# Kernel tuning notes

Measured on AMD Instinct MI355X. Metric: run time of the kernel, lower is better.

Reference implementation:

```python
import jax, jax.numpy as jnp
import numpy as np

N = 50000   # nodes per domain graph
E = 800000  # edges per graph (avg degree 16)
IN = 512    # in_feats
H = 256     # n_hidden
C = 10      # n_classes
ALPHA = 1.0


def setup_inputs() -> dict:
    key = jax.random.key(0)
    ks = jax.random.split(key, 16)
    inp = {
        "features_s": jax.random.normal(ks[0], (N, IN), jnp.float32),
        "labels_s": jax.random.randint(ks[1], (N,), 0, C, jnp.int32),
        "features_t": jax.random.normal(ks[2], (N, IN), jnp.float32),
        "src_s": jax.random.randint(ks[3], (E,), 0, N, jnp.int32),
        "dst_s": jax.random.randint(ks[4], (E,), 0, N, jnp.int32),
        "src_t": jax.random.randint(ks[5], (E,), 0, N, jnp.int32),
        "dst_t": jax.random.randint(ks[6], (E,), 0, N, jnp.int32),
        # GraphConv layer 0: in_feats -> n_hidden (glorot-ish init)
        "W0": jax.random.normal(ks[7], (IN, H), jnp.float32) / np.float32(np.sqrt(IN)),
        "b0": jnp.zeros((H,), jnp.float32),
        # GraphConv layer 1: n_hidden -> n_hidden
        "W1": jax.random.normal(ks[8], (H, H), jnp.float32) / np.float32(np.sqrt(H)),
        "b1": jnp.zeros((H,), jnp.float32),
        # fc head: n_hidden -> n_classes
        "Wfc": jax.random.normal(ks[9], (H, C), jnp.float32) / np.float32(np.sqrt(H)),
        "bfc": jnp.zeros((C,), jnp.float32),
        # JS discriminator: (n_hidden*n_layers + n_classes) -> 2
        "Wd": jax.random.normal(ks[10], (H * 2 + C, 2), jnp.float32) / np.float32(np.sqrt(H * 2 + C)),
        "bd": jnp.zeros((2,), jnp.float32),
    }
    return inp


def _gconv(x, src, dst, W, b, n):
    # DGL GraphConv with norm='both': out = D_in^{-1/2} A D_out^{-1/2} x W + b, then relu.
    ones = jnp.ones(src.shape, x.dtype)
    deg_out = jax.ops.segment_sum(ones, src, num_segments=n)
    deg_in = jax.ops.segment_sum(ones, dst, num_segments=n)
    norm_src = jnp.maximum(deg_out, 1.0) ** -0.5   # [n]
    norm_dst = jnp.maximum(deg_in, 1.0) ** -0.5    # [n]
    h = (x * norm_src[:, None]) @ W                # [n, out] (mult-first: row scaling commutes)
    agg = jax.ops.segment_sum(h[src], dst, num_segments=n)  # gather-scatter SpMM
    return jax.nn.relu(agg * norm_dst[:, None] + b)


def reference(features_s, labels_s, features_t, src_s, dst_s, src_t, dst_t,
              W0, b0, W1, b1, Wfc, bfc, Wd, bd):
    # dropout omitted (eval-mode determinism)
    hs, ht = features_s, features_t
    s_list, t_list = [], []
    for (W, b) in ((W0, b0), (W1, b1)):
        hs = _gconv(hs, src_s, dst_s, W, b, N)
        ht = _gconv(ht, src_t, dst_t, W, b, N)
        s_list.append(hs)
        t_list.append(ht)
    logits_s = hs @ Wfc + bfc
    logits_t = ht @ Wfc + bfc
    s_list.append(logits_s)
    t_list.append(logits_t)

    # class loss: nll over log_softmax
    logp = jax.nn.log_softmax(logits_s, axis=-1)
    class_loss = -jnp.mean(jnp.take_along_axis(logp, labels_s[:, None].astype(jnp.int32), axis=1))

    # JS domain loss with gradient-reversal (identity in forward)
    s_f = jnp.concatenate(s_list, axis=1)  # [N, 2H+C]
    t_f = jnp.concatenate(t_list, axis=1)
    both = jnp.concatenate([s_f, t_f], axis=0)  # [2N, 2H+C]
    rev = -ALPHA * both + jax.lax.stop_gradient((1.0 + ALPHA) * both)  # GRL trick
    dlogits = rev @ Wd + bd
    dlogp = jax.nn.log_softmax(dlogits, axis=-1)
    dlabels = jnp.concatenate([jnp.zeros((N,), jnp.int32), jnp.ones((N,), jnp.int32)])
    domain_loss = -jnp.mean(jnp.take_along_axis(dlogp, dlabels[:, None], axis=1))

    return class_loss + 0.01 * domain_loss
```

## Files before the change

### kernel.cpp

```cpp
#include <hip/hip_runtime.h>
#include <cstdint>
#include <cstddef>

#define NN 50000
#define NNP 50016
#define EE 800000
#define INF 512
#define HH  256
#define CC  10
#define NB2 391
#define NTB 782
#define GB64 782
#define SPMM_BLOCKS 1600
#define HBIN 6250
#define HRNG 8
#define HSUB 32
#define SCAP 1536
#define ZROW NN
#define CAST_TOT (INF * HH + HH * HH + 16 * HH + 16 * HH)

using bfrag = __attribute__((ext_vector_type(8))) __bf16;
using f32x4 = __attribute__((ext_vector_type(4))) float;
using f32x2 = __attribute__((ext_vector_type(2))) float;

__device__ inline unsigned short f2bf(float x) {
    unsigned u = __builtin_bit_cast(unsigned, x);
    unsigned r = u + 0x7FFFu + ((u >> 16) & 1u);
    return (unsigned short)(r >> 16);
}
__device__ inline float bf2f(unsigned short h) {
    return __builtin_bit_cast(float, (unsigned)h << 16);
}

__device__ inline void gload_lds16(const void* gsrc, void* ldst) {
    __builtin_amdgcn_global_load_lds(
        (const __attribute__((address_space(1))) void*)gsrc,
        (__attribute__((address_space(3))) void*)ldst, 16, 0, 0);
}

__global__ void k_cast_all(const float* __restrict__ W0, const float* __restrict__ W1,
                           const float* __restrict__ Wfc, const float* __restrict__ Wd,
                           ushort* __restrict__ W0t, ushort* __restrict__ W1t,
                           ushort* __restrict__ Wt1, ushort* __restrict__ Wt2) {
    int idx = blockIdx.x * blockDim.x + threadIdx.x;
    if (idx < INF * HH) {
        int n = idx / INF, k = idx % INF;
        W0t[idx] = f2bf(W0[(size_t)k * HH + n]);
    } else if (idx < INF * HH + HH * HH) {
        int j = idx - INF * HH;
        int n = j / HH, k = j % HH;
        W1t[j] = f2bf(W1[(size_t)k * HH + n]);
    } else if (idx < INF * HH + HH * HH + 16 * HH) {
        int j = idx - INF * HH - HH * HH;
        int n = j >> 8, k = j & 255;
        float v = 0.f;
        if (n < 10)       v = Wfc[(size_t)k * 10 + n];
        else if (n < 12)  v = Wd[(size_t)(HH + k) * 2 + (n - 10)];
        Wt1[j] = f2bf(v);
    } else if (idx < CAST_TOT) {
        int j = idx - INF * HH - HH * HH - 16 * HH;
        int n = j >> 8, k = j & 255;
        float v = (n < 2) ? Wd[(size_t)k * 2 + n] : 0.f;
        Wt2[j] = f2bf(v);
    }
}

__global__ __launch_bounds__(256) void k_deghist(
        const int* __restrict__ src_s, const int* __restrict__ dst_s,
        const int* __restrict__ src_t, const int* __restrict__ dst_t,
        ushort* __restrict__ pcnt) {
    __shared__ int hist[HBIN];
    const int task = blockIdx.x >> 5;
    const int sub  = blockIdx.x & 31;
    const int arr = task >> 3, range = task & 7;
    const int* p = (arr == 0) ? src_s : (arr == 1) ? dst_s : (arr == 2) ? src_t : dst_t;
    const int4* p4 = reinterpret_cast<const int4*>(p);
    const int lo = range * HBIN;
    for (int j = threadIdx.x; j < HBIN; j += 256) hist[j] = 0;
    __syncthreads();
    for (int i = sub * 256 + (int)threadIdx.x; i < EE / 4; i += HSUB * 256) {
        int4 v = p4[i];
        int a0 = v.x - lo, a1 = v.y - lo, a2 = v.z - lo, a3 = v.w - lo;
        if ((unsigned)a0 < (unsigned)HBIN) atomicAdd(&hist[a0], 1);
        if ((unsigned)a1 < (unsigned)HBIN) atomicAdd(&hist[a1], 1);
        if ((unsigned)a2 < (unsigned)HBIN) atomicAdd(&hist[a2], 1);
        if ((unsigned)a3 < (unsigned)HBIN) atomicAdd(&hist[a3], 1);
    }
    __syncthreads();
    ushort* out = pcnt + ((size_t)task * HSUB + sub) * HBIN;
    for (int j = threadIdx.x; j < HBIN; j += 256) out[j] = (ushort)hist[j];
}

__global__ void k_degsum(const ushort* __restrict__ pcnt, int* __restrict__ cnt) {
    int g = blockIdx.x * blockDim.x + threadIdx.x;
    if (g >= 4 * NN) return;
    int arr = g / NN;
    int node = g - arr * NN;
    int range = node / HBIN;
    int j = node - range * HBIN;
    const ushort* p = pcnt + ((size_t)(arr * HRNG + range) * HSUB) * HBIN + j;
    int s = 0;
    #pragma unroll
    for (int k = 0; k < HSUB; ++k) s += p[(size_t)k * HBIN];
    cnt[g] = s;
}

__global__ void k_scan_blk(const int* __restrict__ cnt, int* __restrict__ off,
                           int* __restrict__ btot) {
    __shared__ int wsum[4];
    int tid = threadIdx.x, lane = tid & 63, wid = tid >> 6;
    int i = blockIdx.x * 256 + tid;
    int v = 0;
    if (i < 2 * NN) v = (i < NN) ? cnt[NN + i] : cnt[2 * NN + i];
    int s = v;
    #pragma unroll
    for (int o = 1; o < 64; o <<= 1) {
        int t = __shfl_up(s, o, 64);
        if (lane >= o) s += t;
    }
    if (lane == 63) wsum[wid] = s;
    __syncthreads();
    if (tid == 0) {
        int a = 0;
        #pragma unroll
        for (int w2 = 0; w2 < 4; ++w2) { int t = wsum[w2]; wsum[w2] = a; a += t; }
        btot[blockIdx.x] = a;
    }
    __syncthreads();
    if (i < 2 * NN) off[i] = wsum[wid] + s - v;
}

__global__ void k_scan_tops(const int* __restrict__ btot, int* __restrict__ bbase,
                            int* __restrict__ off) {
    __shared__ int wsum[8];
    int tid = threadIdx.x, lane = tid & 63, wid = tid >> 6;
    int v = (tid < NB2) ? btot[tid] : 0;
    int s = v;
    #pragma unroll
    for (int o = 1; o < 64; o <<= 1) {
        int t = __shfl_up(s, o, 64);
        if (lane >= o) s += t;
    }
    if (lane == 63) wsum[wid] = s;
    __syncthreads();
    if (tid == 0) {
        int a = 0;
        #pragma unroll
        for (int w2 = 0; w2 < 8; ++w2) { int t = wsum[w2]; wsum[w2] = a; a += t; }
        off[2 * NN] = a;
    }
    __syncthreads();
    if (tid < NB2) bbase[tid] = wsum[wid] + s - v;
}

__global__ void k_scan_fin(int* __restrict__ off, const int* __restrict__ bbase,
                           const int* __restrict__ cnt,
                           float* __restrict__ ns, float* __restrict__ nd,
                           ushort* __restrict__ y2,
                           const ushort* __restrict__ pcnt, int* __restrict__ base2) {
    if (blockIdx.x == 0) {
        #pragma unroll
        for (int j = 0; j < 2; ++j) {
            int idx = j * 256 + (int)threadIdx.x;
            int gg = idx >> 8, grp = (idx >> 5) & 7, c = idx & 31;
            y2[(((size_t)gg * 8 + grp) * NNP + ZROW) * 32 + c] = 0;
        }
    }
    int i = blockIdx.x * blockDim.x + threadIdx.x;
    if (i >= 2 * NN) return;
    int o = off[i] + bbase[i >> 8];
    off[i] = o;
    int co = (i < NN) ? cnt[i] : cnt[NN + i];
    int ci = (i < NN) ? cnt[NN + i] : cnt[2 * NN + i];
    ns[i] = 1.0f / sqrtf(fmaxf((float)co, 1.0f));
    nd[i] = 1.0f / sqrtf(fmaxf((float)ci, 1.0f));
    int g = (i < NN) ? 0 : 1;
    int node = i - g * NN;
    int range = node / HBIN;
    int bin = node - range * HBIN;
    int arr = g ? 3 : 1;
    const ushort* p = pcnt + ((size_t)(arr * HRNG + range) * HSUB) * HBIN + bin;
    int* b = base2 + ((size_t)(g * HRNG + range) * HSUB) * HBIN + bin;
    int run = o;
    #pragma unroll
    for (int s = 0; s < HSUB; ++s) {
        b[(size_t)s * HBIN] = run;
        run += p[(size_t)s * HBIN];
    }
}

__global__ __launch_bounds__(256) void k_fill3(
        const int* __restrict__ src_s, const int* __restrict__ dst_s,
        const int* __restrict__ src_t, const int* __restrict__ dst_t,
        const int* __restrict__ base2, int* __restrict__ csr_src) {
    __shared__ int cur[HBIN];
    const int combo = blockIdx.x & 15;
    const int sub = blockIdx.x >> 4;
    const int g = combo >> 3, range = combo & 7;
    const int4* d4 = reinterpret_cast<const int4*>(g ? dst_t : dst_s);
    const int4* s4 = reinterpret_cast<const int4*>(g ? src_t : src_s);
    const int lo = range * HBIN;
    const int* b = base2 + (size_t)combo * HSUB * HBIN + (size_t)sub * HBIN;
    for (int j = threadIdx.x; j < HBIN; j += 256) cur[j] = b[j];
    __syncthreads();
    for (int i = sub * 256 + (int)threadIdx.x; i < EE / 4; i += HSUB * 256) {
        int4 d = d4[i];
        int b0 = d.x - lo, b1 = d.y - lo, b2 = d.z - lo, b3 = d.w - lo;
        bool o0 = (unsigned)b0 < (unsigned)HBIN;
        bool o1 = (unsigned)b1 < (unsigned)HBIN;
        bool o2 = (unsigned)b2 < (unsigned)HBIN;
        bool o3 = (unsigned)b3 < (unsigned)HBIN;
        if (o0 | o1 | o2 | o3) {
            int4 s = s4[i];
            if (o0) csr_src[atomicAdd(&cur[b0], 1)] = s.x;
            if (o1) csr_src[atomicAdd(&cur[b1], 1)] = s.y;
            if (o2) csr_src[atomicAdd(&cur[b2], 1)] = s.z;
            if (o3) csr_src[atomicAdd(&cur[b3], 1)] = s.w;
        }
    }
}

template<int K, bool F32A>
__global__ __launch_bounds__(256, 4) void k_gemm2(
        const void* __restrict__ Ap_s, const void* __restrict__ Ap_t,
        const ushort* __restrict__ Bt, const float* __restrict__ ns2,
        ushort* __restrict__ y2) {
    __shared__ ushort As[64 * 64];
    __shared__ ushort Bs[256 * 64];
    const int g = blockIdx.x >= GB64 ? 1 : 0;
    const void* Ap = g ? Ap_t : Ap_s;
    const float* ns = ns2 + (size_t)g * NN;
    ushort* y2g = y2 + (size_t)g * 8 * NNP * 32;
    const int m0 = (blockIdx.x - g * GB64) * 64;
    const int t = threadIdx.x;
    const int wid = t >> 6, lane = t & 63;
    const int wc = wid * 64;
    const int l15 = lane & 15, lg = lane >> 4;

    f32x4 acc[4][4];
    #pragma unroll
    for (int m = 0; m < 4; ++m)
        #pragma unroll
        for (int n = 0; n < 4; ++n)
            acc[m][n] = {0.f, 0.f, 0.f, 0.f};

    const int srow = t >> 3;
    const int schunk = t & 7;

    for (int k0 = 0; k0 < K; k0 += 64) {
        if constexpr (F32A) {
            #pragma unroll
            for (int i = 0; i < 2; ++i) {
                int row = srow + i * 32;
                int sw = ((schunk ^ (row & 7)) * 8);
                int m = m0 + row; if (m >= NN) m = NN - 1;
                const float* ap = (const float*)Ap + (size_t)m * K + k0 + schunk * 8;
                float4 f0 = *reinterpret_cast<const float4*>(ap);
                float4 f1 = *reinterpret_cast<const float4*>(ap + 4);
                uint4 va;
                va.x = (unsigned)f2bf(f0.x) | ((unsigned)f2bf(f0.y) << 16);
                va.y = (unsigned)f2bf(f0.z) | ((unsigned)f2bf(f0.w) << 16);
                va.z = (unsigned)f2bf(f1.x) | ((unsigned)f2bf(f1.y) << 16);
                va.w = (unsigned)f2bf(f1.z) | ((unsigned)f2bf(f1.w) << 16);
                *reinterpret_cast<uint4*>(&As[row * 64 + sw]) = va;
            }
        } else {
            #pragma unroll
            for (int i = 0; i < 2; ++i) {
                int row = srow + i * 32;
                int sw = ((schunk ^ (row & 7)) * 8);
                int m = m0 + row; if (m >= NN) m = NN - 1;
                const ushort* gsrc = (const ushort*)Ap + (size_t)m * K + k0 + sw;
                gload_lds16(gsrc, &As[(size_t)(wid * 8 + i * 32) * 64]);
            }
        }
        #pragma unroll
        for (int i = 0; i < 8; ++i) {
            int row = srow + i * 32;
            int sw = ((schunk ^ (row & 7)) * 8);
            const ushort* gsrc = &Bt[(size_t)row * K + k0 + sw];
            gload_lds16(gsrc, &Bs[(size_t)(wid * 8 + i * 32) * 64]);
        }
        __syncthreads();
        #pragma unroll
        for (int kk = 0; kk < 64; kk += 32) {
            const int kc = kk >> 3;
            bfrag af[4];
            #pragma unroll
            for (int m = 0; m < 4; ++m) {
                int row = m * 16 + l15;
                af[m] = *reinterpret_cast<const bfrag*>(&As[row * 64 + (((lg + kc) ^ (row & 7)) * 8)]);
            }
            #pragma unroll
            for (int n = 0; n < 4; ++n) {
                int row = wc + n * 16 + l15;
                bfrag bg = *reinterpret_cast<const bfrag*>(&Bs[row * 64 + (((lg + kc) ^ (row & 7)) * 8)]);
                #pragma unroll
                for (int m = 0; m < 4; ++m)
                    acc[m][n] = __builtin_amdgcn_mfma_f32_16x16x32_bf16(af[m], bg, acc[m][n], 0, 0, 0);
            }
        }
        __syncthreads();
    }

    ushort* tile = Bs;
    #pragma unroll
    for (int m = 0; m < 4; ++m) {
        #pragma unroll
        for (int r = 0; r < 4; ++r) {
            int rloc = m * 16 + lg * 4 + r;
            int rowg = m0 + rloc;
            float nsv = ns[rowg < NN ? rowg : NN - 1];
            #pragma unroll
            for (int n = 0; n < 4; ++n) {
                int col = wc + n * 16 + l15;
                int blk = (col >> 3) ^ (rloc & 7);
                tile[rloc * 256 + (blk << 3) + (col & 7)] = f2bf(acc[m][n][r] * nsv);
            }
        }
    }
    __syncthreads();
    {
        int row = t >> 2, sub = t & 3;
        int m = m0 + row;
        if (m < NN) {
            #pragma unroll
            for (int grp = 0; grp < 8; ++grp) {
                int blk = (grp * 4 + sub) ^ (row & 7);
                uint4 v = *reinterpret_cast<const uint4*>(&tile[row * 256 + (blk << 3)]);
                *reinterpret_cast<uint4*>(&y2g[((size_t)grp * NNP + m) * 32 + sub * 8]) = v;
            }
        }
    }
}

__device__ inline void add8p(f32x2* a, uint4 v) {
    f32x2 p;
    p.x = __builtin_bit_cast(float, v.x << 16);
    p.y = __builtin_bit_cast(float, v.x & 0xffff0000u);
    a[0] += p;
    p.x = __builtin_bit_cast(float, v.y << 16);
    p.y = __builtin_bit_cast(float, v.y & 0xffff0000u);
    a[1] += p;
    p.x = __builtin_bit_cast(float, v.z << 16);
    p.y = __builtin_bit_cast(float, v.z & 0xffff0000u);
    a[2] += p;
    p.x = __builtin_bit_cast(float, v.w << 16);
    p.y = __builtin_bit_cast(float, v.w & 0xffff0000u);
    a[3] += p;
}

__global__ __launch_bounds__(256) void k_spmm7(
        const ushort* __restrict__ y2, const int* __restrict__ off2,
        const int* __restrict__ csr_src, const float* __restrict__ nd2,
        const float* __restrict__ bias, ushort* __restrict__ h_s,
        ushort* __restrict__ h_t) {
    __shared__ int sidx[4][SCAP];
    const int gsel = blockIdx.x >= SPMM_BLOCKS ? 1 : 0;
    const int bid = blockIdx.x - gsel * SPMM_BLOCKS;
    const int* off = off2 + (size_t)gsel * NN;
    const float* nd_arr = nd2 + (size_t)gsel * NN;
    const ushort* y2g = y2 + (size_t)gsel * 8 * NNP * 32;
    ushort* h_out = gsel ? h_t : h_s;

    const int grp = bid & 7;
    const int blk = bid >> 3;
    const int tid = threadIdx.x;
    const int lane = tid & 63, wid = tid >> 6;
    const int slot = lane >> 2;
    const int sub = lane & 3;
    const ushort* ybase = y2g + (size_t)grp * NNP * 32 + sub * 8;

    const int nb = (blk * 4 + wid) * 64;
    int s_wave0 = 0, cnt = 0;
    if (nb < NN) {
        int nend = nb + 64 < NN ? nb + 64 : NN;
        s_wave0 = off[nb];
        cnt = off[nend] - s_wave0;
    }
    int stage = cnt < SCAP ? cnt : SCAP;
    for (int j = lane; j < stage; j += 64)
        sidx[wid][j] = csr_src[s_wave0 + j];
    __syncthreads();

    float bia[8];
    #pragma unroll
    for (int j = 0; j < 8; ++j) bia[j] = bias[grp * 32 + sub * 8 + j];

    int e0[4], e1[4];
    f32x2 a[4][4];
    #pragma unroll
    for (int c = 0; c < 4; ++c) {
        int n = nb + c * 16 + slot;
        bool v = n < NN;
        e0[c] = v ? off[n] - s_wave0 : 0;
        e1[c] = v ? off[n + 1] - s_wave0 : 0;
        #pragma unroll
        for (int j = 0; j < 4; ++j) a[c][j] = {0.f, 0.f};
    }
    int tmax = max(max(e1[0] - e0[0], e1[1] - e0[1]), max(e1[2] - e0[2], e1[3] - e0[3]));

    if (cnt <= SCAP) {
        for (int t = 0; t < tmax; t += 2) {
            uint4 v[8];
            #pragma unroll
            for (int u = 0; u < 2; ++u)
                #pragma unroll
                for (int c = 0; c < 4; ++c) {
                    int ec = e0[c] + t + u;
                    bool val = ec < e1[c];
                    int ecc = val ? ec : 0;
                    int id = sidx[wid][ecc];
                    id = val ? id : ZROW;
                    v[u * 4 + c] = *reinterpret_cast<const uint4*>(&ybase[(size_t)id * 32]);
                }
            #pragma unroll
            for (int u = 0; u < 2; ++u)
                #pragma unroll
                for (int c = 0; c < 4; ++c) add8p(a[c], v[u * 4 + c]);
        }
    } else {
        for (int t = 0; t < tmax; t += 2) {
            uint4 v[8];
            #pragma unroll
            for (int u = 0; u < 2; ++u)
                #pragma unroll
                for (int c = 0; c < 4; ++c) {
                    int ec = e0[c] + t + u;
                    bool val = ec < e1[c];
                    int ecc = val ? ec : 0;
                    int id = csr_src[s_wave0 + ecc];
                    id = val ? id : ZROW;
                    v[u * 4 + c] = *reinterpret_cast<const uint4*>(&ybase[(size_t)id * 32]);
                }
            #pragma unroll
            for (int u = 0; u < 2; ++u)
                #pragma unroll
                for (int c = 0; c < 4; ++c) add8p(a[c], v[u * 4 + c]);
        }
    }

    #pragma unroll
    for (int c = 0; c < 4; ++c) {
        int n = nb + c * 16 + slot;
        if (n >= NN) continue;
        float nd = nd_arr[n];
        ushort r[8];
        #pragma unroll
        for (int j = 0; j < 8; ++j) {
            float av = (j & 1) ? a[c][j >> 1].y : a[c][j >> 1].x;
            r[j] = f2bf(fmaxf(av * nd + bia[j], 0.f));
        }
        uint4 pk;
        pk.x = (unsigned)r[0] | ((unsigned)r[1] << 16);
        pk.y = (unsigned)r[2] | ((unsigned)r[3] << 16);
        pk.z = (unsigned)r[4] | ((unsigned)r[5] << 16);
        pk.w = (unsigned)r[6] | ((unsigned)r[7] << 16);
        *reinterpret_cast<uint4*>(&h_out[(size_t)n * 256 + grp * 32 + sub * 8]) = pk;
    }
}

__global__ __launch_bounds__(256) void k_tail_mfma(
        const ushort* __restrict__ h0s, const ushort* __restrict__ h0t,
        const ushort* __restrict__ h1s, const ushort* __restrict__ h1t,
        const ushort* __restrict__ Wt1, const ushort* __restrict__ Wt2,
        const float* __restrict__ bfc, const float* __restrict__ bd,
        const int* __restrict__ labels,
        float* __restrict__ pcls, float* __restrict__ pdom) {
    __shared__ float sT1[4][16][17];
    __shared__ float sT2[4][16][17];
    __shared__ float sc[4], sd[4];
    const int g = blockIdx.x >= NTB ? 1 : 0;
    const int bi = blockIdx.x - g * NTB;
    const ushort* h0 = g ? h0t : h0s;
    const ushort* h1 = g ? h1t : h1s;
    const int tid = threadIdx.x;
    const int wid = tid >> 6, lane = tid & 63;
    const int l15 = lane & 15, lg = lane >> 4;
    const int base = bi * 64 + wid * 16;

    int arow = base + l15; if (arow >= NN) arow = NN - 1;
    const ushort* a1 = h1 + (size_t)arow * 256 + lg * 8;
    const ushort* a0 = h0 + (size_t)arow * 256 + lg * 8;
    const ushort* b1 = Wt1 + (size_t)l15 * 256 + lg * 8;
    const ushort* b2 = Wt2 + (size_t)l15 * 256 + lg * 8;
    f32x4 acc1 = {0.f, 0.f, 0.f, 0.f};
    f32x4 acc2 = {0.f, 0.f, 0.f, 0.f};
    #pragma unroll
    for (int kk = 0; kk < 8; ++kk) {
        bfrag af1 = *reinterpret_cast<const bfrag*>(a1 + kk * 32);
        bfrag bg1 = *reinterpret_cast<const bfrag*>(b1 + kk * 32);
        acc1 = __builtin_amdgcn_mfma_f32_16x16x32_bf16(af1, bg1, acc1, 0, 0, 0);
        bfrag af0 = *reinterpret_cast<const bfrag*>(a0 + kk * 32);
        bfrag bg2 = *reinterpret_cast<const bfrag*>(b2 + kk * 32);
        acc2 = __builtin_amdgcn_mfma_f32_16x16x32_bf16(af0, bg2, acc2, 0, 0, 0);
    }
    #pragma unroll
    for (int j = 0; j < 4; ++j) {
        sT1[wid][lg * 4 + j][l15] = acc1[j];
        sT2[wid][lg * 4 + j][l15] = acc2[j];
    }
    __syncthreads();

    float cls = 0.f, dom = 0.f;
    int n = base + lane;
    if (lane < 16 && n < NN) {
        float lgt[10];
        #pragma unroll
        for (int c = 0; c < 10; ++c) lgt[c] = sT1[wid][lane][c] + bfc[c];
        float dl0 = bd[0] + sT2[wid][lane][0] + sT1[wid][lane][10];
        float dl1 = bd[1] + sT2[wid][lane][1] + sT1[wid][lane][11];
        if (g == 0) {
            float m = lgt[0];
            #pragma unroll
            for (int c = 1; c < 10; ++c) m = fmaxf(m, lgt[c]);
            float s = 0.f;
            #pragma unroll
            for (int c = 0; c < 10; ++c) s += expf(lgt[c] - m);
            int lab = labels[n];
            float tgt = lgt[0];
            #pragma unroll
            for (int c = 1; c < 10; ++c) tgt = (c == lab) ? lgt[c] : tgt;
            cls = -(tgt - (m + logf(s)));
        }
        float m2 = fmaxf(dl0, dl1);
        float lse2 = m2 + logf(expf(dl0 - m2) + expf(dl1 - m2));
        dom = -((g ? dl1 : dl0) - lse2);
    }
    #pragma unroll
    for (int o = 1; o < 16; o <<= 1) {
        cls += __shfl_xor(cls, o, 64);
        dom += __shfl_xor(dom, o, 64);
    }
    if (lane == 0) { sc[wid] = cls; sd[wid] = dom; }
    __syncthreads();
    if (tid == 0) {
        float c = sc[0] + sc[1] + sc[2] + sc[3];
        float d = sd[0] + sd[1] + sd[2] + sd[3];
        if (g == 0) pcls[bi] = c;
        pdom[g * NTB + bi] = d;
    }
}

__global__ void k_finalize(const float* __restrict__ pcls, const float* __restrict__ pdom,
                           float* __restrict__ out) {
    __shared__ float sc[4], sd[4];
    int tid = threadIdx.x, lane = tid & 63, wid = tid >> 6;
    float c = 0.f, d = 0.f;
    for (int i = tid; i < NTB; i += 256) c += pcls[i];
    for (int i = tid; i < 2 * NTB; i += 256) d += pdom[i];
    #pragma unroll
    for (int o = 32; o; o >>= 1) {
        c += __shfl_xor(c, o, 64);
        d += __shfl_xor(d, o, 64);
    }
    if (lane == 0) { sc[wid] = c; sd[wid] = d; }
    __syncthreads();
    if (tid == 0) {
        float ct = sc[0] + sc[1] + sc[2] + sc[3];
        float dt = sd[0] + sd[1] + sd[2] + sd[3];
        out[0] = ct / (float)NN + 0.01f * (dt / (float)(2 * NN));
    }
}

extern "C" void kernel_launch(void* const* d_in, const int* in_sizes, int n_in,
                              void* d_out, int out_size, void* d_ws, size_t ws_size,
                              hipStream_t stream) {
    const float* features_s = (const float*)d_in[0];
    const int*   labels_s   = (const int*)d_in[1];
    const float* features_t = (const float*)d_in[2];
    const int*   src_s      = (const int*)d_in[3];
    const int*   dst_s      = (const int*)d_in[4];
    const int*   src_t      = (const int*)d_in[5];
    const int*   dst_t      = (const int*)d_in[6];
    const float* W0         = (const float*)d_in[7];
    const float* b0         = (const float*)d_in[8];
    const float* W1         = (const float*)d_in[9];
    const float* b1         = (const float*)d_in[10];
    const float* Wfc        = (const float*)d_in[11];
    const float* bfc        = (const float*)d_in[12];
    const float* Wd         = (const float*)d_in[13];
    const float* bd         = (const float*)d_in[14];
    float* out = (float*)d_out;

    auto align256 = [](size_t x) { return (x + 255) & ~(size_t)255; };
    char* w = (char*)d_ws;
    ushort* h0s    = (ushort*)w; w += align256((size_t)NN * HH * 2);
    ushort* h0t    = (ushort*)w; w += align256((size_t)NN * HH * 2);
    ushort* h1s    = (ushort*)w; w += align256((size_t)NN * HH * 2);
    ushort* h1t    = (ushort*)w; w += align256((size_t)NN * HH * 2);
    ushort* y2     = (ushort*)w; w += align256((size_t)2 * 8 * NNP * 32 * 2);
    ushort* W0t    = (ushort*)w; w += align256((size_t)INF * HH * 2);
    ushort* W1t    = (ushort*)w; w += align256((size_t)HH * HH * 2);
    ushort* Wt1    = (ushort*)w; w += align256((size_t)16 * HH * 2);
    ushort* Wt2    = (ushort*)w; w += align256((size_t)16 * HH * 2);
    float* ns      = (float*)w;  w += align256((size_t)2 * NN * 4);
    float* nd      = (float*)w;  w += align256((size_t)2 * NN * 4);
    int*   cnt     = (int*)w;    w += align256((size_t)4 * NN * 4);
    int*   csr_off = (int*)w;    w += align256((size_t)(2 * NN + 1) * 4);
    int*   csr_src = (int*)w;    w += align256((size_t)2 * EE * 4);
    int*   btot    = (int*)w;    w += align256((size_t)NB2 * 4);
    int*   bbase   = (int*)w;    w += align256((size_t)NB2 * 4);
    float* pcls    = (float*)w;  w += align256((size_t)NTB * 4);
    float* pdom    = (float*)w;  w += align256((size_t)2 * NTB * 4);
    ushort* pcnt   = (ushort*)w; w += align256((size_t)4 * HRNG * HSUB * HBIN * 2);
    int*   base2   = (int*)w;    w += align256((size_t)2 * HRNG * HSUB * HBIN * 4);

    const int TB = 256;
    k_cast_all<<<(CAST_TOT + TB - 1) / TB, TB, 0, stream>>>(W0, W1, Wfc, Wd,
                                                            W0t, W1t, Wt1, Wt2);

    k_deghist<<<4 * HRNG * HSUB, TB, 0, stream>>>(src_s, dst_s, src_t, dst_t, pcnt);
    k_degsum<<<(4 * NN + TB - 1) / TB, TB, 0, stream>>>(pcnt, cnt);
    k_scan_blk<<<NB2, TB, 0, stream>>>(cnt, csr_off, btot);
    k_scan_tops<<<1, 512, 0, stream>>>(btot, bbase, csr_off);
    k_scan_fin<<<NB2, TB, 0, stream>>>(csr_off, bbase, cnt, ns, nd, y2, pcnt, base2);
    k_fill3<<<16 * HSUB, TB, 0, stream>>>(src_s, dst_s, src_t, dst_t, base2, csr_src);

    k_gemm2<INF, true><<<2 * GB64, TB, 0, stream>>>(features_s, features_t, W0t, ns, y2);
    k_spmm7<<<2 * SPMM_BLOCKS, TB, 0, stream>>>(y2, csr_off, csr_src, nd, b0, h0s, h0t);

    k_gemm2<HH, false><<<2 * GB64, TB, 0, stream>>>(h0s, h0t, W1t, ns, y2);
    k_spmm7<<<2 * SPMM_BLOCKS, TB, 0, stream>>>(y2, csr_off, csr_src, nd, b1, h1s, h1t);

    k_tail_mfma<<<2 * NTB, TB, 0, stream>>>(h0s, h0t, h1s, h1t, Wt1, Wt2, bfc, bd,
                                            labels_s, pcls, pdom);
    k_finalize<<<1, TB, 0, stream>>>(pcls, pdom, out);
}
```

Measured before the change: 395.7 us.

## Stagger source/target domain GEMM and SpMM into fused heterogeneous launches

Instead of running each GEMM and SpMM over both domains at once, the pipeline is shifted by one domain. Each launch now runs the SpMM of one domain alongside the GEMM of the other, in a single kernel where the block index picks the body. The aim is to overlap compute-bound MFMA GEMM work with memory-bound gather SpMM work on the same GPU. The cost is five launches instead of four, a shared-memory footprint sized for the larger GEMM body, and 4-blocks-per-CU launch bounds now also applied to the SpMM blocks.

```diff
diff --git a/kernel.cpp b/kernel.cpp
--- a/kernel.cpp
+++ b/kernel.cpp
@@ -18,6 +18,7 @@
 #define SCAP 1536
 #define ZROW NN
 #define CAST_TOT (INF * HH + HH * HH + 16 * HH + 16 * HH)
+#define SMEM_BYTES 40960
 
 using bfrag = __attribute__((ext_vector_type(8))) __bf16;
 using f32x4 = __attribute__((ext_vector_type(4))) float;
@@ -221,17 +222,11 @@
 }
 
 template<int K, bool F32A>
-__global__ __launch_bounds__(256, 4) void k_gemm2(
-        const void* __restrict__ Ap_s, const void* __restrict__ Ap_t,
-        const ushort* __restrict__ Bt, const float* __restrict__ ns2,
-        ushort* __restrict__ y2) {
-    __shared__ ushort As[64 * 64];
-    __shared__ ushort Bs[256 * 64];
-    const int g = blockIdx.x >= GB64 ? 1 : 0;
-    const void* Ap = g ? Ap_t : Ap_s;
-    const float* ns = ns2 + (size_t)g * NN;
-    ushort* y2g = y2 + (size_t)g * 8 * NNP * 32;
-    const int m0 = (blockIdx.x - g * GB64) * 64;
+__device__ __forceinline__ void gemm_body(
+        char* smem, const void* __restrict__ Ap, const ushort* __restrict__ Bt,
+        const float* __restrict__ ns, ushort* __restrict__ y2g, int m0) {
+    ushort* As = reinterpret_cast<ushort*>(smem);
+    ushort* Bs = reinterpret_cast<ushort*>(smem + 8192);
     const int t = threadIdx.x;
     const int wid = t >> 6, lane = t & 63;
     const int wc = wid * 64;
@@ -334,7 +329,7 @@
     }
 }
 
-__device__ inline void add8p(f32x2* a, uint4 v) {
+__device__ __forceinline__ void add8p(f32x2* a, uint4 v) {
     f32x2 p;
     p.x = __builtin_bit_cast(float, v.x << 16);
     p.y = __builtin_bit_cast(float, v.x & 0xffff0000u);
@@ -350,19 +345,11 @@
     a[3] += p;
 }
 
-__global__ __launch_bounds__(256) void k_spmm7(
-        const ushort* __restrict__ y2, const int* __restrict__ off2,
-        const int* __restrict__ csr_src, const float* __restrict__ nd2,
-        const float* __restrict__ bias, ushort* __restrict__ h_s,
-        ushort* __restrict__ h_t) {
-    __shared__ int sidx[4][SCAP];
-    const int gsel = blockIdx.x >= SPMM_BLOCKS ? 1 : 0;
-    const int bid = blockIdx.x - gsel * SPMM_BLOCKS;
-    const int* off = off2 + (size_t)gsel * NN;
-    const float* nd_arr = nd2 + (size_t)gsel * NN;
-    const ushort* y2g = y2 + (size_t)gsel * 8 * NNP * 32;
-    ushort* h_out = gsel ? h_t : h_s;
-
+__device__ __forceinline__ void spmm_body(
+        char* smem, const ushort* __restrict__ y2g, const int* __restrict__ off,
+        const int* __restrict__ csr_src, const float* __restrict__ nd_arr,
+        const float* __restrict__ bias, ushort* __restrict__ h_out, int bid) {
+    int (*sidx)[SCAP] = reinterpret_cast<int (*)[SCAP]>(smem);
     const int grp = bid & 7;
     const int blk = bid >> 3;
     const int tid = threadIdx.x;
@@ -457,6 +444,37 @@
         pk.z = (unsigned)r[4] | ((unsigned)r[5] << 16);
         pk.w = (unsigned)r[6] | ((unsigned)r[7] << 16);
         *reinterpret_cast<uint4*>(&h_out[(size_t)n * 256 + grp * 32 + sub * 8]) = pk;
+    }
+}
+
+template<int K, bool F32A>
+__global__ __launch_bounds__(256, 4) void k_gemm1(
+        const void* __restrict__ Ap, const ushort* __restrict__ Bt,
+        const float* __restrict__ ns, ushort* __restrict__ y2g) {
+    __shared__ __align__(16) char smem[SMEM_BYTES];
+    gemm_body<K, F32A>(smem, Ap, Bt, ns, y2g, blockIdx.x * 64);
+}
+
+__global__ __launch_bounds__(256) void k_spmm1(
+        const ushort* __restrict__ y2g, const int* __restrict__ off,
+        const int* __restrict__ csr_src, const float* __restrict__ nd_arr,
+        const float* __restrict__ bias, ushort* __restrict__ h_out) {
+    __shared__ __align__(16) char smem[24576];
+    spmm_body(smem, y2g, off, csr_src, nd_arr, bias, h_out, blockIdx.x);
+}
+
+template<int K, bool F32A>
+__global__ __launch_bounds__(256, 4) void k_fused(
+        const ushort* __restrict__ y2_sp, const int* __restrict__ off_sp,
+        const int* __restrict__ csr_src, const float* __restrict__ nd_sp,
+        const float* __restrict__ bias, ushort* __restrict__ h_out,
+        const void* __restrict__ Ag, const ushort* __restrict__ Bt,
+        const float* __restrict__ ns_g, ushort* __restrict__ y2_g) {
+    __shared__ __align__(16) char smem[SMEM_BYTES];
+    if (blockIdx.x < SPMM_BLOCKS) {
+        spmm_body(smem, y2_sp, off_sp, csr_src, nd_sp, bias, h_out, blockIdx.x);
+    } else {
+        gemm_body<K, F32A>(smem, Ag, Bt, ns_g, y2_g, (blockIdx.x - SPMM_BLOCKS) * 64);
     }
 }
 
@@ -617,11 +635,22 @@
     k_scan_fin<<<NB2, TB, 0, stream>>>(csr_off, bbase, cnt, ns, nd, y2, pcnt, base2);
     k_fill3<<<16 * HSUB, TB, 0, stream>>>(src_s, dst_s, src_t, dst_t, base2, csr_src);
 
-    k_gemm2<INF, true><<<2 * GB64, TB, 0, stream>>>(features_s, features_t, W0t, ns, y2);
-    k_spmm7<<<2 * SPMM_BLOCKS, TB, 0, stream>>>(y2, csr_off, csr_src, nd, b0, h0s, h0t);
-
-    k_gemm2<HH, false><<<2 * GB64, TB, 0, stream>>>(h0s, h0t, W1t, ns, y2);
-    k_spmm7<<<2 * SPMM_BLOCKS, TB, 0, stream>>>(y2, csr_off, csr_src, nd, b1, h1s, h1t);
+    const int* off_s = csr_off;
+    const int* off_t = csr_off + NN;
+    ushort* y2s = y2;
+    ushort* y2t = y2 + (size_t)8 * NNP * 32;
+
+    k_gemm1<INF, true><<<GB64, TB, 0, stream>>>(features_s, W0t, ns, y2s);
+    k_fused<INF, true><<<SPMM_BLOCKS + GB64, TB, 0, stream>>>(
+        y2s, off_s, csr_src, nd, b0, h0s,
+        features_t, W0t, ns + NN, y2t);
+    k_fused<HH, false><<<SPMM_BLOCKS + GB64, TB, 0, stream>>>(
+        y2t, off_t, csr_src, nd + NN, b0, h0t,
+        h0s, W1t, ns, y2s);
+    k_fused<HH, false><<<SPMM_BLOCKS + GB64, TB, 0, stream>>>(
+        y2s, off_s, csr_src, nd, b1, h1s,
+        h0t, W1t, ns + NN, y2t);
+    k_spmm1<<<SPMM_BLOCKS, TB, 0, stream>>>(y2t, off_t, csr_src, nd + NN, b1, h1t);
 
     k_tail_mfma<<<2 * NTB, TB, 0, stream>>>(h0s, h0t, h1s, h1t, Wt1, Wt2, bfc, bd,
                                             labels_s, pcls, pdom);
```

New measurement: 401.5 us. Within noise of the previous version (+1.5%).
